# Kernel optimization log

Hardware: AMD Instinct MI355X
Metric: run time of the kernel (lower is better)

The kernel has to match this reference:

```python
import jax, jax.numpy as jnp
import numpy as np

BLOCK = 512
WINDOW = 2
NEG = -1e9


def _pad_to_block(x, block):
    pad_len = (-x.shape[1]) % block
    if pad_len:
        x = jnp.pad(x, ((0, 0), (0, pad_len), (0, 0)))
    return x


def setup_inputs() -> dict:
    key = jax.random.key(0)
    ks = jax.random.split(key, 8)
    B, Lq, Lk, C = 2, 8192, 8192, 128
    s = 1.0 / np.sqrt(C)
    return {
        "query": jax.random.normal(ks[0], (B, Lq, C), jnp.float32),
        "key_value": jax.random.normal(ks[1], (B, Lk, C), jnp.float32),
        "Wq": jax.random.normal(ks[2], (C, C), jnp.float32) * s,
        "bq": jax.random.normal(ks[3], (C,), jnp.float32) * 0.01,
        "Wkv": jax.random.normal(ks[4], (C, 2 * C), jnp.float32) * s,
        "bkv": jax.random.normal(ks[5], (2 * C,), jnp.float32) * 0.01,
        "Wo": jax.random.normal(ks[6], (C, C), jnp.float32) * s,
        "bo": jax.random.normal(ks[7], (C,), jnp.float32) * 0.01,
    }


def reference(query, key_value, Wq, bq, Wkv, bkv, Wo, bo):
    B, Lq, C = query.shape
    qp = _pad_to_block(query, BLOCK)
    kp = _pad_to_block(key_value, BLOCK)
    q = qp @ Wq + bq                      # [B, Lq_pad, C]
    kv = kp @ Wkv + bkv                   # [B, Lk_pad, 2C]
    k, v = kv[..., :C], kv[..., C:]
    nq = qp.shape[1] // BLOCK
    nk = kp.shape[1] // BLOCK
    qb = q.reshape(B, nq, BLOCK, C)
    kb = k.reshape(B, nk, BLOCK, C)
    vb = v.reshape(B, nk, BLOCK, C)
    allowed = jnp.abs(jnp.arange(nq)[:, None] - jnp.arange(nk)[None, :]) <= WINDOW  # [nq, nk]
    # scores: [B, nq, nk, s, d] with s = q-pos in block, d = k-pos in block
    scores = jnp.einsum('bqsc,bkdc->bqksd', qb, kb) / jnp.sqrt(jnp.asarray(C, qb.dtype))
    scores = jnp.where(allowed[None, :, :, None, None], scores, NEG)
    # NOTE: faithful to original torch code, softmax over axis=3 (the 's' axis)
    attn = jax.nn.softmax(scores, axis=3)
    out = jnp.einsum('bqksd,bkdc->bqsc', attn, vb)
    out = out.reshape(B, nq * BLOCK, C)[:, :Lq]
    return out @ Wo + bo
```

## Files before the change

kernel.cpp:

```cpp
#include <hip/hip_runtime.h>

typedef _Float16 f16;
typedef _Float16 half8 __attribute__((ext_vector_type(8)));
typedef float floatx4 __attribute__((ext_vector_type(4)));

#define MFMA16(a,b,c) __builtin_amdgcn_mfma_f32_16x16x32_f16((a),(b),(c),0,0,0)
#define RSL2E 0.12751743f

__device__ __forceinline__ void split2(float x, f16 &h, f16 &l) {
  f16 hh = (f16)x;
  h = hh;
  l = (f16)(x - (float)hh);
}

__device__ __forceinline__ void stage_rows64(const f16* __restrict__ g, int gstride,
                                             f16* lds, int rows, int tid, int nthr) {
  int total = rows * 8;
  for (int idx = tid; idx < total; idx += nthr) {
    int row = idx >> 3, slot = idx & 7;
    float4 v = *(const float4*)(g + (size_t)row * gstride + slot * 8);
    int lofs = ((row << 7) + (slot << 4)) ^ ((row & 7) << 4);
    *(float4*)((char*)lds + lofs) = v;
  }
}
__device__ __forceinline__ void stage_rows128(const f16* __restrict__ g, int gstride,
                                              f16* lds, int rows, int tid, int nthr) {
  int total = rows * 16;
  for (int idx = tid; idx < total; idx += nthr) {
    int row = idx >> 4, slot = idx & 15;
    float4 v = *(const float4*)(g + (size_t)row * gstride + slot * 8);
    int lofs = ((row << 8) + (slot << 4)) ^ ((row & 7) << 4);
    *(float4*)((char*)lds + lofs) = v;
  }
}
__device__ __forceinline__ half8 fragP128(const f16* lds, int row, int kofs) {
  int ofs = ((row << 7) + (kofs << 1)) ^ ((row & 7) << 4);
  return *(const half8*)((const char*)lds + ofs);
}
__device__ __forceinline__ half8 fragP256(const f16* lds, int row, int kofs) {
  int ofs = ((row << 8) + (kofs << 1)) ^ ((row & 7) << 4);
  return *(const half8*)((const char*)lds + ofs);
}
__device__ __forceinline__ void pack_split(float4 v, uint2 &h, uint2 &l) {
  union { f16 a[4]; uint2 u; } hh, ll;
  split2(v.x, hh.a[0], ll.a[0]);
  split2(v.y, hh.a[1], ll.a[1]);
  split2(v.z, hh.a[2], ll.a[2]);
  split2(v.w, hh.a[3], ll.a[3]);
  h = hh.u; l = ll.u;
}

__global__ void k_splitW(const float* __restrict__ Wq, const float* __restrict__ Wkv,
                         const float* __restrict__ Wo,
                         f16* WqTh, f16* WqTl, f16* WkvTh, f16* WkvTl,
                         f16* WoTh, f16* WoTl) {
  int idx = blockIdx.x * 256 + threadIdx.x;
  if (idx >= 65536) return;
  float v; f16 *ph, *pl; int dst;
  if (idx < 16384) {
    int n = idx >> 7, c = idx & 127;
    v = Wq[c * 128 + n]; ph = WqTh; pl = WqTl; dst = idx;
  } else if (idx < 49152) {
    int t = idx - 16384; int n = t >> 7, c = t & 127;
    v = Wkv[c * 256 + n]; ph = WkvTh; pl = WkvTl; dst = t;
  } else {
    int t = idx - 49152; int n = t >> 7, c = t & 127;
    v = Wo[c * 128 + n]; ph = WoTh; pl = WoTl; dst = t;
  }
  f16 h, l; split2(v, h, l);
  ph[dst] = h; pl[dst] = l;
}

__global__ __launch_bounds__(512, 2)
void k_proj(const float* __restrict__ query, const float* __restrict__ key_value,
            const f16* __restrict__ WqTh, const f16* __restrict__ WqTl,
            const f16* __restrict__ WkvTh, const f16* __restrict__ WkvTl,
            const float* __restrict__ bq, const float* __restrict__ bkv,
            f16* __restrict__ qhp, f16* __restrict__ khp, f16* __restrict__ vT) {
  int pidx = blockIdx.x >> 8, blk = blockIdx.x & 255;
  const float* A; const f16 *BTh, *BTl; const float* bias; f16* out; int mode;
  if (pidx == 0)      { A = query;     BTh = WqTh;          BTl = WqTl;          bias = bq;        out = qhp; mode = 0; }
  else if (pidx == 1) { A = key_value; BTh = WkvTh;         BTl = WkvTl;         bias = bkv;       out = khp; mode = 0; }
  else                { A = key_value; BTh = WkvTh + 16384; BTl = WkvTl + 16384; bias = bkv + 128; out = vT;  mode = 1; }
  __shared__ f16 pool[24576];
  f16* sAh = pool;
  f16* sAl = pool + 4096;
  f16* sBh = pool + 8192;
  f16* sBl = pool + 16384;
  int tid = threadIdx.x, wave = tid >> 6, lane = tid & 63, lg = lane >> 4, lr = lane & 15;
  int wm = wave >> 2, wn = wave & 3;
  size_t rowbase = (size_t)blk * 64;
  int arow = tid >> 4, acg = tid & 15;
  int al0 = ((arow << 7) + (acg << 3)) ^ ((arow & 7) << 4);
  int al1 = (((arow + 32) << 7) + (acg << 3)) ^ ((arow & 7) << 4);
  int brow = tid >> 3, bslot = tid & 7;
  int bl0 = ((brow << 7) + (bslot << 4)) ^ ((brow & 7) << 4);
  int bl1 = (((brow + 64) << 7) + (bslot << 4)) ^ ((brow & 7) << 4);
  const float* Ab = A + rowbase * 128;
  float4 a0 = *(const float4*)(Ab + (size_t)arow * 128 + acg * 4);
  float4 a1 = *(const float4*)(Ab + (size_t)(arow + 32) * 128 + acg * 4);
  float4 b0h = *(const float4*)(BTh + brow * 128 + bslot * 8);
  float4 b1h = *(const float4*)(BTh + (brow + 64) * 128 + bslot * 8);
  float4 b0l = *(const float4*)(BTl + brow * 128 + bslot * 8);
  float4 b1l = *(const float4*)(BTl + (brow + 64) * 128 + bslot * 8);
  floatx4 zero = {0.f, 0.f, 0.f, 0.f};
  floatx4 acc[2][2] = {{zero, zero}, {zero, zero}};
  #pragma unroll
  for (int cc = 0; cc < 128; cc += 64) {
    __syncthreads();
    {
      uint2 h, l;
      pack_split(a0, h, l);
      *(uint2*)((char*)sAh + al0) = h; *(uint2*)((char*)sAl + al0) = l;
      pack_split(a1, h, l);
      *(uint2*)((char*)sAh + al1) = h; *(uint2*)((char*)sAl + al1) = l;
    }
    *(float4*)((char*)sBh + bl0) = b0h;
    *(float4*)((char*)sBh + bl1) = b1h;
    *(float4*)((char*)sBl + bl0) = b0l;
    *(float4*)((char*)sBl + bl1) = b1l;
    __syncthreads();
    if (cc == 0) {
      a0 = *(const float4*)(Ab + (size_t)arow * 128 + 64 + acg * 4);
      a1 = *(const float4*)(Ab + (size_t)(arow + 32) * 128 + 64 + acg * 4);
      b0h = *(const float4*)(BTh + 64 + brow * 128 + bslot * 8);
      b1h = *(const float4*)(BTh + 64 + (brow + 64) * 128 + bslot * 8);
      b0l = *(const float4*)(BTl + 64 + brow * 128 + bslot * 8);
      b1l = *(const float4*)(BTl + 64 + (brow + 64) * 128 + bslot * 8);
    }
    #pragma unroll
    for (int kc = 0; kc < 64; kc += 32) {
      half8 ah[2], al[2];
      for (int fm = 0; fm < 2; fm++) {
        ah[fm] = fragP128(sAh, wm * 32 + fm * 16 + lr, kc + lg * 8);
        al[fm] = fragP128(sAl, wm * 32 + fm * 16 + lr, kc + lg * 8);
      }
      for (int fn = 0; fn < 2; fn++) {
        half8 bh = fragP128(sBh, wn * 32 + fn * 16 + lr, kc + lg * 8);
        half8 bl = fragP128(sBl, wn * 32 + fn * 16 + lr, kc + lg * 8);
        for (int fm = 0; fm < 2; fm++) {
          acc[fm][fn] = MFMA16(ah[fm], bh, acc[fm][fn]);
          acc[fm][fn] = MFMA16(ah[fm], bl, acc[fm][fn]);
          acc[fm][fn] = MFMA16(al[fm], bh, acc[fm][fn]);
        }
      }
    }
  }
  __syncthreads();
  f16* e = pool;
  for (int fm = 0; fm < 2; fm++) for (int fn = 0; fn < 2; fn++) {
    int n = wn * 32 + fn * 16 + lr;
    float bs = bias[n];
    for (int jj = 0; jj < 4; jj++) {
      int m = wm * 32 + fm * 16 + lg * 4 + jj;
      e[m * 136 + n] = (f16)(acc[fm][fn][jj] + bs);
    }
  }
  __syncthreads();
  if (mode == 0) {
    for (int idx = tid; idx < 1024; idx += 512) {
      int r = idx >> 4, sl = idx & 15;
      *(float4*)(out + (rowbase + r) * 128 + sl * 8) =
          *(const float4*)((const char*)e + r * 272 + sl * 16);
    }
  } else {
    size_t bidx = rowbase >> 13, lofs = rowbase & 8191;
    for (int idx = tid; idx < 1024; idx += 512) {
      int c = idx >> 3, sl = idx & 7;
      union { f16 a[8]; float4 v; } th;
      for (int t = 0; t < 8; t++) th.a[t] = e[(sl * 8 + t) * 136 + c];
      *(float4*)(out + (bidx * 128 + c) * 8192 + lofs + sl * 8) = th.v;
    }
  }
}

__global__ __launch_bounds__(512, 2)
void k_final(const float* __restrict__ Pbuf, const float* __restrict__ U,
             const f16* __restrict__ BTh, const f16* __restrict__ BTl,
             const float* __restrict__ bias, float* __restrict__ out) {
  __shared__ f16 pool[24576];
  f16* sAh = pool;
  f16* sAl = pool + 4096;
  f16* sBh = pool + 8192;
  f16* sBl = pool + 16384;
  int tid = threadIdx.x, wave = tid >> 6, lane = tid & 63, lg = lane >> 4, lr = lane & 15;
  int wm = wave >> 2, wn = wave & 3;
  size_t rowbase = (size_t)blockIdx.x * 64;
  int b = (int)(rowbase >> 13), r0 = (int)(rowbase & 8191);
  int i = r0 >> 9, st = (r0 >> 6) & 7;
  const float* p0 = Pbuf + ((size_t)(((b * 16 + i) * 8 + st) * 4)) * 8192;
  const float* p1 = p0 + 8192;
  const float* p2 = p0 + 16384;
  const float* p3 = p0 + 24576;
  const float* Ub = U + ((size_t)b * 16 + i) * 128;
  int arow = tid >> 4, acg = tid & 15;
  int al0 = ((arow << 7) + (acg << 3)) ^ ((arow & 7) << 4);
  int al1 = (((arow + 32) << 7) + (acg << 3)) ^ ((arow & 7) << 4);
  int brow = tid >> 3, bslot = tid & 7;
  int bl0 = ((brow << 7) + (bslot << 4)) ^ ((brow & 7) << 4);
  int bl1 = (((brow + 64) << 7) + (bslot << 4)) ^ ((brow & 7) << 4);
  int c0 = acg * 4;
  float4 r0a0 = *(const float4*)(p0 + arow * 128 + c0);
  float4 r0a1 = *(const float4*)(p1 + arow * 128 + c0);
  float4 r0a2 = *(const float4*)(p2 + arow * 128 + c0);
  float4 r0a3 = *(const float4*)(p3 + arow * 128 + c0);
  float4 r1a0 = *(const float4*)(p0 + (arow + 32) * 128 + c0);
  float4 r1a1 = *(const float4*)(p1 + (arow + 32) * 128 + c0);
  float4 r1a2 = *(const float4*)(p2 + (arow + 32) * 128 + c0);
  float4 r1a3 = *(const float4*)(p3 + (arow + 32) * 128 + c0);
  float4 uu = *(const float4*)(Ub + c0);
  float4 b0h = *(const float4*)(BTh + brow * 128 + bslot * 8);
  float4 b1h = *(const float4*)(BTh + (brow + 64) * 128 + bslot * 8);
  float4 b0l = *(const float4*)(BTl + brow * 128 + bslot * 8);
  float4 b1l = *(const float4*)(BTl + (brow + 64) * 128 + bslot * 8);
  floatx4 zero = {0.f, 0.f, 0.f, 0.f};
  floatx4 acc[2][2] = {{zero, zero}, {zero, zero}};
  #pragma unroll
  for (int cc = 0; cc < 128; cc += 64) {
    __syncthreads();
    {
      float4 s0, s1;
      s0.x = (r0a0.x + r0a1.x) + (r0a2.x + r0a3.x) + uu.x;
      s0.y = (r0a0.y + r0a1.y) + (r0a2.y + r0a3.y) + uu.y;
      s0.z = (r0a0.z + r0a1.z) + (r0a2.z + r0a3.z) + uu.z;
      s0.w = (r0a0.w + r0a1.w) + (r0a2.w + r0a3.w) + uu.w;
      s1.x = (r1a0.x + r1a1.x) + (r1a2.x + r1a3.x) + uu.x;
      s1.y = (r1a0.y + r1a1.y) + (r1a2.y + r1a3.y) + uu.y;
      s1.z = (r1a0.z + r1a1.z) + (r1a2.z + r1a3.z) + uu.z;
      s1.w = (r1a0.w + r1a1.w) + (r1a2.w + r1a3.w) + uu.w;
      uint2 h, l;
      pack_split(s0, h, l);
      *(uint2*)((char*)sAh + al0) = h; *(uint2*)((char*)sAl + al0) = l;
      pack_split(s1, h, l);
      *(uint2*)((char*)sAh + al1) = h; *(uint2*)((char*)sAl + al1) = l;
    }
    *(float4*)((char*)sBh + bl0) = b0h;
    *(float4*)((char*)sBh + bl1) = b1h;
    *(float4*)((char*)sBl + bl0) = b0l;
    *(float4*)((char*)sBl + bl1) = b1l;
    __syncthreads();
    if (cc == 0) {
      int c1 = 64 + acg * 4;
      r0a0 = *(const float4*)(p0 + arow * 128 + c1);
      r0a1 = *(const float4*)(p1 + arow * 128 + c1);
      r0a2 = *(const float4*)(p2 + arow * 128 + c1);
      r0a3 = *(const float4*)(p3 + arow * 128 + c1);
      r1a0 = *(const float4*)(p0 + (arow + 32) * 128 + c1);
      r1a1 = *(const float4*)(p1 + (arow + 32) * 128 + c1);
      r1a2 = *(const float4*)(p2 + (arow + 32) * 128 + c1);
      r1a3 = *(const float4*)(p3 + (arow + 32) * 128 + c1);
      uu   = *(const float4*)(Ub + c1);
      b0h = *(const float4*)(BTh + 64 + brow * 128 + bslot * 8);
      b1h = *(const float4*)(BTh + 64 + (brow + 64) * 128 + bslot * 8);
      b0l = *(const float4*)(BTl + 64 + brow * 128 + bslot * 8);
      b1l = *(const float4*)(BTl + 64 + (brow + 64) * 128 + bslot * 8);
    }
    #pragma unroll
    for (int kc = 0; kc < 64; kc += 32) {
      half8 ah[2], al[2];
      for (int fm = 0; fm < 2; fm++) {
        ah[fm] = fragP128(sAh, wm * 32 + fm * 16 + lr, kc + lg * 8);
        al[fm] = fragP128(sAl, wm * 32 + fm * 16 + lr, kc + lg * 8);
      }
      for (int fn = 0; fn < 2; fn++) {
        half8 bh = fragP128(sBh, wn * 32 + fn * 16 + lr, kc + lg * 8);
        half8 bl = fragP128(sBl, wn * 32 + fn * 16 + lr, kc + lg * 8);
        for (int fm = 0; fm < 2; fm++) {
          acc[fm][fn] = MFMA16(ah[fm], bh, acc[fm][fn]);
          acc[fm][fn] = MFMA16(ah[fm], bl, acc[fm][fn]);
          acc[fm][fn] = MFMA16(al[fm], bh, acc[fm][fn]);
        }
      }
    }
  }
  __syncthreads();
  float* ef = (float*)pool;
  for (int fm = 0; fm < 2; fm++) for (int fn = 0; fn < 2; fn++) {
    int n = wn * 32 + fn * 16 + lr;
    float bs = bias[n];
    for (int jj = 0; jj < 4; jj++) {
      int m = wm * 32 + fm * 16 + lg * 4 + jj;
      ef[m * 132 + n] = acc[fm][fn][jj] + bs;
    }
  }
  __syncthreads();
  for (int idx = tid; idx < 2048; idx += 512) {
    int r = idx >> 5, sl = idx & 31;
    *(float4*)(out + (rowbase + r) * 128 + sl * 4) = *(const float4*)(ef + r * 132 + sl * 4);
  }
}

__global__ void k_U(const f16* __restrict__ vT, float* __restrict__ U) {
  int b = blockIdx.x >> 7, c = blockIdx.x & 127;
  int tid = threadIdx.x;
  const f16* r = vT + ((size_t)b * 128 + c) * 8192;
  float s = 0.f;
  const float4* r4 = (const float4*)(r + tid * 32);
  for (int t = 0; t < 4; t++) {
    float4 v = r4[t];
    const f16* a = (const f16*)&v;
    for (int u = 0; u < 8; u++) s += (float)a[u];
  }
  __shared__ float part[256];
  __shared__ float bs[16];
  part[tid] = s;
  __syncthreads();
  if (tid < 16) {
    float t = 0.f;
    for (int u = 0; u < 16; u++) t += part[tid * 16 + u];
    bs[tid] = t;
  }
  __syncthreads();
  if (tid < 16) {
    int i = tid;
    float tot = 0.f;
    for (int j = 0; j < 16; j++) tot += bs[j];
    int j0 = i - 2 < 0 ? 0 : i - 2;
    int j1 = i + 2 > 15 ? 15 : i + 2;
    float win = 0.f;
    for (int j = j0; j <= j1; j++) win += bs[j];
    U[((size_t)b * 16 + i) * 128 + c] = (tot - win) * (1.0f / 512.0f);
  }
}

__global__ __launch_bounds__(512, 4)
void k_passA(const f16* __restrict__ kp, const f16* __restrict__ qp,
             float* __restrict__ Z) {
  int bid = blockIdx.x;
  int wg = (bid & 7) * 80 + (bid >> 3);
  int dchunk = wg & 3; int rest = wg >> 2;
  int slot = rest % 5; int rest2 = rest / 5;
  int i = rest2 & 15; int b = rest2 >> 4;
  int j = i - 2 + slot;
  if (j < 0 || j > 15) return;
  __shared__ f16 sK[16384], sQ[16384];
  int tid = threadIdx.x, wave = tid >> 6, lane = tid & 63, lg = lane >> 4, lr = lane & 15;
  int wm = wave >> 1, wn = wave & 1;
  size_t krow = (size_t)b * 8192 + j * 512 + dchunk * 128;
  stage_rows128(kp + krow * 128, 128, sK, 128, tid, 512);
  int qr = tid >> 4, qsl = tid & 15;
  int ql0 = ((qr << 8) + (qsl << 4)) ^ ((qr & 7) << 4);
  int ql1 = (((qr + 32) << 8) + (qsl << 4)) ^ ((qr & 7) << 4);
  int ql2 = (((qr + 64) << 8) + (qsl << 4)) ^ ((qr & 7) << 4);
  int ql3 = (((qr + 96) << 8) + (qsl << 4)) ^ ((qr & 7) << 4);
  const f16* qb = qp + ((size_t)b * 8192 + i * 512) * 128;
  float4 q0 = *(const float4*)(qb + (size_t)(qr      ) * 128 + qsl * 8);
  float4 q1 = *(const float4*)(qb + (size_t)(qr +  32) * 128 + qsl * 8);
  float4 q2 = *(const float4*)(qb + (size_t)(qr +  64) * 128 + qsl * 8);
  float4 q3 = *(const float4*)(qb + (size_t)(qr +  96) * 128 + qsl * 8);
  float zp[2][4] = {{0.f,0.f,0.f,0.f},{0.f,0.f,0.f,0.f}};
  floatx4 zero = {0.f, 0.f, 0.f, 0.f};
  for (int sc = 0; sc < 4; sc++) {
    __syncthreads();
    *(float4*)((char*)sQ + ql0) = q0;
    *(float4*)((char*)sQ + ql1) = q1;
    *(float4*)((char*)sQ + ql2) = q2;
    *(float4*)((char*)sQ + ql3) = q3;
    __syncthreads();
    if (sc < 3) {
      const f16* qn = qb + (size_t)(sc + 1) * 128 * 128;
      q0 = *(const float4*)(qn + (size_t)(qr      ) * 128 + qsl * 8);
      q1 = *(const float4*)(qn + (size_t)(qr +  32) * 128 + qsl * 8);
      q2 = *(const float4*)(qn + (size_t)(qr +  64) * 128 + qsl * 8);
      q3 = *(const float4*)(qn + (size_t)(qr +  96) * 128 + qsl * 8);
    }
    floatx4 acc[2][4] = {{zero,zero,zero,zero},{zero,zero,zero,zero}};
    for (int kc = 0; kc < 128; kc += 32) {
      half8 ah[2];
      for (int fm = 0; fm < 2; fm++)
        ah[fm] = fragP256(sK, wm * 32 + fm * 16 + lr, kc + lg * 8);
      for (int fn = 0; fn < 4; fn++) {
        half8 bh = fragP256(sQ, wn * 64 + fn * 16 + lr, kc + lg * 8);
        for (int fm = 0; fm < 2; fm++)
          acc[fm][fn] = MFMA16(ah[fm], bh, acc[fm][fn]);
      }
    }
    for (int fm = 0; fm < 2; fm++) for (int fn = 0; fn < 4; fn++)
      for (int jj = 0; jj < 4; jj++)
        zp[fm][jj] += exp2f(acc[fm][fn][jj] * RSL2E);
  }
  for (int off = 1; off < 16; off <<= 1)
    for (int fm = 0; fm < 2; fm++) for (int jj = 0; jj < 4; jj++)
      zp[fm][jj] += __shfl_xor(zp[fm][jj], off, 64);
  __syncthreads();
  float* sred = (float*)sQ;
  if (lr == 0) {
    for (int fm = 0; fm < 2; fm++) for (int jj = 0; jj < 4; jj++) {
      int d = wm * 32 + fm * 16 + lg * 4 + jj;
      sred[wn * 128 + d] = zp[fm][jj];
    }
  }
  __syncthreads();
  if (tid < 128) {
    size_t zb = (((size_t)(b * 16 + i) * 16 + j) * 512) + dchunk * 128;
    Z[zb + tid] = sred[tid] + sred[128 + tid];
  }
}

__global__ __launch_bounds__(512, 4)
void k_passB(const f16* __restrict__ qp, const f16* __restrict__ kp,
             const f16* __restrict__ vT,
             const float* __restrict__ Z, float* __restrict__ Pbuf) {
  int bid = blockIdx.x;
  int wg = ((bid & 7) << 7) | (bid >> 3);
  int dq = wg & 3, st = (wg >> 2) & 7, i = (wg >> 5) & 15, b = wg >> 9;
  __shared__ __align__(16) char pool[65536];
  f16* sQ  = (f16*)pool;
  f16* sKV = (f16*)(pool + 16384);
  f16* sE  = (f16*)(pool + 49152);
  int tid = threadIdx.x, wave = tid >> 6, lane = tid & 63, lg = lane >> 4, lr = lane & 15;
  int w1m = wave >> 1, w1n = wave & 1;
  int w2m = wave >> 2, w2n = wave & 3;
  int srow = tid >> 4, sslot = tid & 15;
  int sl0 = (((srow      ) << 8) + (sslot << 4)) ^ ((srow & 7) << 4);
  int sl1 = (((srow +  32) << 8) + (sslot << 4)) ^ ((srow & 7) << 4);
  int sl2 = (((srow +  64) << 8) + (sslot << 4)) ^ ((srow & 7) << 4);
  int sl3 = (((srow +  96) << 8) + (sslot << 4)) ^ ((srow & 7) << 4);
  size_t qrow = (size_t)b * 8192 + i * 512 + st * 64;
  stage_rows128(qp + qrow * 128, 128, sQ, 64, tid, 512);
  floatx4 zero = {0.f, 0.f, 0.f, 0.f};
  floatx4 acc2[2][2] = {{zero, zero}, {zero, zero}};
  const f16* vbase = vT + (size_t)b * 1048576;
  for (int slot = 0; slot < 5; slot++) {
    int j = i - 2 + slot;
    if (j < 0 || j > 15) continue;
    const f16* kb = kp + ((size_t)b * 8192 + j * 512 + dq * 128) * 128;
    float4 k0 = *(const float4*)(kb + (size_t)(srow      ) * 128 + sslot * 8);
    float4 k1 = *(const float4*)(kb + (size_t)(srow +  32) * 128 + sslot * 8);
    float4 k2 = *(const float4*)(kb + (size_t)(srow +  64) * 128 + sslot * 8);
    float4 k3 = *(const float4*)(kb + (size_t)(srow +  96) * 128 + sslot * 8);
    const f16* gv = vbase + (size_t)j * 512 + dq * 128;
    float4 v0 = *(const float4*)(gv + (size_t)(srow      ) * 8192 + sslot * 8);
    float4 v1 = *(const float4*)(gv + (size_t)(srow +  32) * 8192 + sslot * 8);
    float4 v2 = *(const float4*)(gv + (size_t)(srow +  64) * 8192 + sslot * 8);
    float4 v3 = *(const float4*)(gv + (size_t)(srow +  96) * 8192 + sslot * 8);
    float rz[2][4];
    {
      size_t zb = (((size_t)(b * 16 + i) * 16 + j) * 512) + dq * 128;
      #pragma unroll
      for (int fm = 0; fm < 2; fm++)
        #pragma unroll
        for (int jj = 0; jj < 4; jj++)
          rz[fm][jj] = 1.0f / Z[zb + w1m * 32 + fm * 16 + lg * 4 + jj];
    }
    __syncthreads();
    *(float4*)((char*)sKV + sl0) = k0;
    *(float4*)((char*)sKV + sl1) = k1;
    *(float4*)((char*)sKV + sl2) = k2;
    *(float4*)((char*)sKV + sl3) = k3;
    __syncthreads();
    floatx4 acc1[2][2] = {{zero, zero}, {zero, zero}};
    #pragma unroll
    for (int kc = 0; kc < 128; kc += 32) {
      half8 ah0 = fragP256(sKV, w1m * 32 + lr, kc + lg * 8);
      half8 ah1 = fragP256(sKV, w1m * 32 + 16 + lr, kc + lg * 8);
      #pragma unroll
      for (int fn = 0; fn < 2; fn++) {
        half8 bq = fragP256(sQ, w1n * 32 + fn * 16 + lr, kc + lg * 8);
        acc1[0][fn] = MFMA16(ah0, bq, acc1[0][fn]);
        acc1[1][fn] = MFMA16(ah1, bq, acc1[1][fn]);
      }
    }
    __syncthreads();
    #pragma unroll
    for (int fm = 0; fm < 2; fm++)
      #pragma unroll
      for (int fn = 0; fn < 2; fn++) {
        int s = w1n * 32 + fn * 16 + lr;
        int d0 = w1m * 32 + fm * 16 + lg * 4;
        union { f16 a[4]; float2 u; } pk;
        #pragma unroll
        for (int jj = 0; jj < 4; jj++)
          pk.a[jj] = (f16)(exp2f(acc1[fm][fn][jj] * RSL2E) * rz[fm][jj]);
        int ofs = ((s << 8) + (d0 << 1)) ^ ((s & 7) << 4);
        *(float2*)((char*)sE + ofs) = pk.u;
      }
    *(float4*)((char*)sKV + sl0) = v0;
    *(float4*)((char*)sKV + sl1) = v1;
    *(float4*)((char*)sKV + sl2) = v2;
    *(float4*)((char*)sKV + sl3) = v3;
    __syncthreads();
    #pragma unroll
    for (int kc = 0; kc < 128; kc += 32) {
      half8 ea0 = fragP256(sE, w2m * 32 + lr, kc + lg * 8);
      half8 ea1 = fragP256(sE, w2m * 32 + 16 + lr, kc + lg * 8);
      #pragma unroll
      for (int fn = 0; fn < 2; fn++) {
        half8 bh = fragP256(sKV, w2n * 32 + fn * 16 + lr, kc + lg * 8);
        acc2[0][fn] = MFMA16(ea0, bh, acc2[0][fn]);
        acc2[1][fn] = MFMA16(ea1, bh, acc2[1][fn]);
      }
    }
  }
  __syncthreads();
  float* ef = (float*)pool;
  for (int fm = 0; fm < 2; fm++) for (int fn = 0; fn < 2; fn++) {
    int c = w2n * 32 + fn * 16 + lr;
    for (int jj = 0; jj < 4; jj++) {
      int s = w2m * 32 + fm * 16 + lg * 4 + jj;
      ef[s * 128 + c] = acc2[fm][fn][jj];
    }
  }
  __syncthreads();
  float* po = Pbuf + ((size_t)((((b * 16 + i) * 8 + st) * 4) + dq)) * 8192;
  for (int idx = tid; idx < 2048; idx += 512)
    ((float4*)po)[idx] = ((const float4*)ef)[idx];
}

extern "C" void kernel_launch(void* const* d_in, const int* in_sizes, int n_in,
                              void* d_out, int out_size, void* d_ws, size_t ws_size,
                              hipStream_t stream) {
  const float* query     = (const float*)d_in[0];
  const float* key_value = (const float*)d_in[1];
  const float* Wq  = (const float*)d_in[2];
  const float* bq  = (const float*)d_in[3];
  const float* Wkv = (const float*)d_in[4];
  const float* bkv = (const float*)d_in[5];
  const float* Wo  = (const float*)d_in[6];
  const float* bo  = (const float*)d_in[7];
  float* out = (float*)d_out;

  char* ws = (char*)d_ws;
  size_t off = 0;
  auto alloc = [&](size_t bytes) -> char* {
    char* p = ws + off;
    off += (bytes + 255) & ~(size_t)255;
    return p;
  };
  const size_t SZH = (size_t)16384 * 128 * 2;
  f16* qhp  = (f16*)alloc(SZH);
  f16* khp  = (f16*)alloc(SZH);
  f16* vT   = (f16*)alloc(SZH);
  float* Pbuf = (float*)alloc((size_t)1024 * 8192 * 4);
  f16* WqTh  = (f16*)alloc(32768); f16* WqTl  = (f16*)alloc(32768);
  f16* WkvTh = (f16*)alloc(65536); f16* WkvTl = (f16*)alloc(65536);
  f16* WoTh  = (f16*)alloc(32768); f16* WoTl  = (f16*)alloc(32768);
  float* Zb = (float*)alloc((size_t)2 * 16 * 16 * 512 * 4);
  float* Ub = (float*)alloc((size_t)2 * 16 * 128 * 4);
  if (off > ws_size) return;

  k_splitW<<<256, 256, 0, stream>>>(Wq, Wkv, Wo, WqTh, WqTl, WkvTh, WkvTl, WoTh, WoTl);
  k_proj<<<768, 512, 0, stream>>>(query, key_value, WqTh, WqTl, WkvTh, WkvTl,
                                  bq, bkv, qhp, khp, vT);
  k_U<<<256, 256, 0, stream>>>(vT, Ub);
  k_passA<<<640, 512, 0, stream>>>(khp, qhp, Zb);
  k_passB<<<1024, 512, 0, stream>>>(qhp, khp, vT, Zb, Pbuf);
  k_final<<<256, 512, 0, stream>>>(Pbuf, Ub, WoTh, WoTl, bo, out);
}
```

Measured before the change: 106.1 us.

## Prefetch next K/V/Z block into registers during current iteration; pad epilogue LDS

```diff
diff --git a/kernel.cpp b/kernel.cpp
--- a/kernel.cpp
+++ b/kernel.cpp
@@ -421,28 +421,24 @@
   floatx4 zero = {0.f, 0.f, 0.f, 0.f};
   floatx4 acc2[2][2] = {{zero, zero}, {zero, zero}};
   const f16* vbase = vT + (size_t)b * 1048576;
-  for (int slot = 0; slot < 5; slot++) {
-    int j = i - 2 + slot;
-    if (j < 0 || j > 15) continue;
-    const f16* kb = kp + ((size_t)b * 8192 + j * 512 + dq * 128) * 128;
-    float4 k0 = *(const float4*)(kb + (size_t)(srow      ) * 128 + sslot * 8);
-    float4 k1 = *(const float4*)(kb + (size_t)(srow +  32) * 128 + sslot * 8);
-    float4 k2 = *(const float4*)(kb + (size_t)(srow +  64) * 128 + sslot * 8);
-    float4 k3 = *(const float4*)(kb + (size_t)(srow +  96) * 128 + sslot * 8);
-    const f16* gv = vbase + (size_t)j * 512 + dq * 128;
-    float4 v0 = *(const float4*)(gv + (size_t)(srow      ) * 8192 + sslot * 8);
-    float4 v1 = *(const float4*)(gv + (size_t)(srow +  32) * 8192 + sslot * 8);
-    float4 v2 = *(const float4*)(gv + (size_t)(srow +  64) * 8192 + sslot * 8);
-    float4 v3 = *(const float4*)(gv + (size_t)(srow +  96) * 8192 + sslot * 8);
-    float rz[2][4];
-    {
-      size_t zb = (((size_t)(b * 16 + i) * 16 + j) * 512) + dq * 128;
-      #pragma unroll
-      for (int fm = 0; fm < 2; fm++)
-        #pragma unroll
-        for (int jj = 0; jj < 4; jj++)
-          rz[fm][jj] = 1.0f / Z[zb + w1m * 32 + fm * 16 + lg * 4 + jj];
-    }
+  int j0 = i - 2 < 0 ? 0 : i - 2, j1 = i + 2 > 15 ? 15 : i + 2;
+  const f16* kb0 = kp + ((size_t)b * 8192 + j0 * 512 + dq * 128) * 128;
+  float4 k0 = *(const float4*)(kb0 + (size_t)(srow      ) * 128 + sslot * 8);
+  float4 k1 = *(const float4*)(kb0 + (size_t)(srow +  32) * 128 + sslot * 8);
+  float4 k2 = *(const float4*)(kb0 + (size_t)(srow +  64) * 128 + sslot * 8);
+  float4 k3 = *(const float4*)(kb0 + (size_t)(srow +  96) * 128 + sslot * 8);
+  const f16* gv0 = vbase + (size_t)j0 * 512 + dq * 128;
+  float4 v0 = *(const float4*)(gv0 + (size_t)(srow      ) * 8192 + sslot * 8);
+  float4 v1 = *(const float4*)(gv0 + (size_t)(srow +  32) * 8192 + sslot * 8);
+  float4 v2 = *(const float4*)(gv0 + (size_t)(srow +  64) * 8192 + sslot * 8);
+  float4 v3 = *(const float4*)(gv0 + (size_t)(srow +  96) * 8192 + sslot * 8);
+  const float* zp0 = Z + (((size_t)(b * 16 + i) * 16 + j0) * 512) + dq * 128 + w1m * 32 + lg * 4;
+  float4 za = *(const float4*)(zp0);
+  float4 zb4 = *(const float4*)(zp0 + 16);
+  for (int j = j0; j <= j1; j++) {
+    float4 ra, rb;
+    ra.x = 1.0f / za.x;  ra.y = 1.0f / za.y;  ra.z = 1.0f / za.z;  ra.w = 1.0f / za.w;
+    rb.x = 1.0f / zb4.x; rb.y = 1.0f / zb4.y; rb.z = 1.0f / zb4.z; rb.w = 1.0f / zb4.w;
     __syncthreads();
     *(float4*)((char*)sKV + sl0) = k0;
     *(float4*)((char*)sKV + sl1) = k1;
@@ -469,9 +465,10 @@
         int s = w1n * 32 + fn * 16 + lr;
         int d0 = w1m * 32 + fm * 16 + lg * 4;
         union { f16 a[4]; float2 u; } pk;
-        #pragma unroll
-        for (int jj = 0; jj < 4; jj++)
-          pk.a[jj] = (f16)(exp2f(acc1[fm][fn][jj] * RSL2E) * rz[fm][jj]);
+        pk.a[0] = (f16)(exp2f(acc1[fm][fn][0] * RSL2E) * (fm ? rb.x : ra.x));
+        pk.a[1] = (f16)(exp2f(acc1[fm][fn][1] * RSL2E) * (fm ? rb.y : ra.y));
+        pk.a[2] = (f16)(exp2f(acc1[fm][fn][2] * RSL2E) * (fm ? rb.z : ra.z));
+        pk.a[3] = (f16)(exp2f(acc1[fm][fn][3] * RSL2E) * (fm ? rb.w : ra.w));
         int ofs = ((s << 8) + (d0 << 1)) ^ ((s & 7) << 4);
         *(float2*)((char*)sE + ofs) = pk.u;
       }
@@ -479,6 +476,21 @@
     *(float4*)((char*)sKV + sl1) = v1;
     *(float4*)((char*)sKV + sl2) = v2;
     *(float4*)((char*)sKV + sl3) = v3;
+    if (j < j1) {
+      const f16* nkb = kp + ((size_t)b * 8192 + (j + 1) * 512 + dq * 128) * 128;
+      k0 = *(const float4*)(nkb + (size_t)(srow      ) * 128 + sslot * 8);
+      k1 = *(const float4*)(nkb + (size_t)(srow +  32) * 128 + sslot * 8);
+      k2 = *(const float4*)(nkb + (size_t)(srow +  64) * 128 + sslot * 8);
+      k3 = *(const float4*)(nkb + (size_t)(srow +  96) * 128 + sslot * 8);
+      const f16* ngv = vbase + (size_t)(j + 1) * 512 + dq * 128;
+      v0 = *(const float4*)(ngv + (size_t)(srow      ) * 8192 + sslot * 8);
+      v1 = *(const float4*)(ngv + (size_t)(srow +  32) * 8192 + sslot * 8);
+      v2 = *(const float4*)(ngv + (size_t)(srow +  64) * 8192 + sslot * 8);
+      v3 = *(const float4*)(ngv + (size_t)(srow +  96) * 8192 + sslot * 8);
+      const float* nzp = Z + (((size_t)(b * 16 + i) * 16 + (j + 1)) * 512) + dq * 128 + w1m * 32 + lg * 4;
+      za = *(const float4*)(nzp);
+      zb4 = *(const float4*)(nzp + 16);
+    }
     __syncthreads();
     #pragma unroll
     for (int kc = 0; kc < 128; kc += 32) {
@@ -498,13 +510,15 @@
     int c = w2n * 32 + fn * 16 + lr;
     for (int jj = 0; jj < 4; jj++) {
       int s = w2m * 32 + fm * 16 + lg * 4 + jj;
-      ef[s * 128 + c] = acc2[fm][fn][jj];
+      ef[s * 132 + c] = acc2[fm][fn][jj];
     }
   }
   __syncthreads();
   float* po = Pbuf + ((size_t)((((b * 16 + i) * 8 + st) * 4) + dq)) * 8192;
-  for (int idx = tid; idx < 2048; idx += 512)
-    ((float4*)po)[idx] = ((const float4*)ef)[idx];
+  for (int idx = tid; idx < 2048; idx += 512) {
+    int r = idx >> 5, sl = idx & 31;
+    *(float4*)(po + r * 128 + sl * 4) = *(const float4*)(ef + r * 132 + sl * 4);
+  }
 }
 
 extern "C" void kernel_launch(void* const* d_in, const int* in_sizes, int n_in,
```

Result: slower. 144.2 us (+35.9%).
